# Optimization experiments

Measured on AMD Instinct MI355X. Metric: run time of the kernel, lower is better.

## Reference

```python
import jax, jax.numpy as jnp
import numpy as np
from jax import lax

N, C, H, W = 8, 512, 28, 28
G = 8                     # attention groups
QKP = 32                  # qk_planes = out/groups/2
VP = 64                   # v_planes = branch/groups
BP = 512                  # branch_planes
HW = H * W
EPS = 1e-5                # BatchNorm eps (eval mode, running_mean=0, running_var=1)


def bn(x, gamma, beta, axis=1):
    shape = [1] * x.ndim
    shape[axis] = x.shape[axis]
    g = gamma.reshape(shape)
    b = beta.reshape(shape)
    return x * (g / jnp.sqrt(1.0 + EPS)) + b


def conv2d(x, w, groups=1):
    return lax.conv_general_dilated(
        x, w, (1, 1), 'SAME',
        dimension_numbers=('NCHW', 'OIHW', 'NCHW'),
        feature_group_count=groups)


def setup_inputs() -> dict:
    key = jax.random.key(0)
    ks = jax.random.split(key, 16)
    pe_dim = 2 * QKP + VP  # 128
    inp = {
        'x':        jax.random.normal(ks[0], (N, C, H, W), jnp.float32),
        'qkv_w':    jax.random.normal(ks[1], (BP * 2, C), jnp.float32) * np.sqrt(1.0 / C),
        'g_qkv':    jax.random.normal(ks[2], (BP * 2,), jnp.float32) * 0.1 + 1.0,
        'b_qkv':    jax.random.normal(ks[3], (BP * 2,), jnp.float32) * 0.1,
        'g_sim':    jax.random.normal(ks[4], (G * 3,), jnp.float32) * 0.1 + 1.0,
        'b_sim':    jax.random.normal(ks[5], (G * 3,), jnp.float32) * 0.1,
        'g_out':    jax.random.normal(ks[6], (BP * 2,), jnp.float32) * 0.1 + 1.0,
        'b_out':    jax.random.normal(ks[7], (BP * 2,), jnp.float32) * 0.1,
        'relative': jax.random.normal(ks[8], (pe_dim, 2 * HW - 1), jnp.float32) * np.sqrt(1.0 / VP),
        'xw1':      jax.random.normal(ks[9], (BP, C // G, 3, 3), jnp.float32) * np.sqrt(2.0 / (C // G * 9)),
        'xw2':      jax.random.normal(ks[10], (BP, BP, 1, 1), jnp.float32) * np.sqrt(2.0 / BP),
        'g_x':      jnp.ones((BP,), jnp.float32),
        'b_x':      jnp.zeros((BP,), jnp.float32),
        'rw':       jax.random.normal(ks[11], (BP, BP * 2, 1, 1), jnp.float32) * np.sqrt(2.0 / (BP * 2)),
        'g_r':      jnp.ones((BP,), jnp.float32),
        'b_r':      jnp.zeros((BP,), jnp.float32),
        'pw':       jax.random.normal(ks[12], (BP, BP, 1, 1), jnp.float32) * np.sqrt(2.0 / BP),
        'g_p':      jnp.ones((BP,), jnp.float32),
        'b_p':      jnp.zeros((BP,), jnp.float32),
    }
    return inp


def reference(x, qkv_w, g_qkv, b_qkv, g_sim, b_sim, g_out, b_out, relative,
              xw1, xw2, g_x, b_x, rw, g_r, b_r, pw, g_p, b_p):
    n = x.shape[0]
    # ---- unary branch: grouped 3x3 conv + 1x1 conv + BN ----
    unary = conv2d(x, xw1, groups=G)
    unary = conv2d(unary, xw2)
    unary = bn(unary, g_x, b_x)

    # ---- binary branch (attention over HW tokens) ----
    xf = x.reshape(n, C, HW)
    qkv = jnp.einsum('oc,bci->boi', qkv_w, xf)          # Conv1d k=1
    qkv = bn(qkv, g_qkv, b_qkv)
    qkv = qkv.reshape(n, G, 2 * QKP + VP, HW)
    q = qkv[:, :, :QKP]
    k = qkv[:, :, QKP:2 * QKP]
    v = qkv[:, :, 2 * QKP:]

    # relative position embeddings via index gather: emb[c,i,j] = relative[c, i-j+HW-1]
    idx = jnp.arange(HW)
    rel_idx = idx[:, None] - idx[None, :] + HW - 1      # [HW, HW]
    emb = relative[:, rel_idx]                           # [pe_dim, HW, HW]
    q_emb, k_emb, v_emb = emb[:QKP], emb[QKP:2 * QKP], emb[2 * QKP:]

    qk = jnp.einsum('bgci,bgcj->bgij', q, k)
    qr = jnp.einsum('bgci,cij->bgij', q, q_emb)
    kr = jnp.einsum('bgci,cij->bgij', k, k_emb).swapaxes(2, 3)
    stacked = jnp.concatenate([qk, qr, kr], axis=1)      # [n, 3G, HW, HW]
    stacked = bn(stacked, g_sim, b_sim)
    logits = stacked.reshape(n, 3, G, HW, HW).sum(axis=1)
    sim = jax.nn.softmax(logits, axis=-1)                # softmax over keys j

    sv = jnp.einsum('bgij,bgcj->bgci', sim, v)
    sve = jnp.einsum('bgij,cij->bgci', sim, v_emb)
    stacked_binary = jnp.concatenate([sv, sve], axis=-1).reshape(n, BP * 2, HW)
    stacked_binary = bn(stacked_binary, g_out, b_out)
    binary = stacked_binary.reshape(n, BP, 2, HW).sum(axis=2).reshape(n, BP, H, W)

    # ---- gating / reasoning path ----
    gate_in = jnp.concatenate([unary, binary], axis=1)   # [n, 2*BP, H, W]
    r = jax.nn.relu(gate_in)
    r = jax.nn.relu(bn(conv2d(r, rw), g_r, b_r))
    gate = jax.nn.sigmoid(bn(conv2d(r, pw), g_p, b_p))

    return gate * binary + unary


if __name__ == '__main__':
    out = reference(**setup_inputs())
    print(out.shape, out.dtype)
```

## Files before the change

### kernel.cpp

```cpp
#include <hip/hip_runtime.h>
#include <math.h>


typedef unsigned short u16;
typedef unsigned int u32;
typedef __bf16 bf16x8 __attribute__((ext_vector_type(8)));
typedef float f32x4 __attribute__((ext_vector_type(4)));

#define INVS 0.99999500003749968f
#define MFMA16(a, b, c) __builtin_amdgcn_mfma_f32_16x16x32_bf16(a, b, c, 0, 0, 0)

__device__ inline u16 f2bf(float f) {
  u32 u = __builtin_bit_cast(u32, f);
  return (u16)((u + 0x7fffu + ((u >> 16) & 1u)) >> 16);
}
__device__ inline bf16x8 ld_bf8(const u16* p) {
  int4 v = *reinterpret_cast<const int4*>(p);
  return __builtin_bit_cast(bf16x8, v);
}
__device__ inline bf16x8 pack8(const u16 h[8]) {
  int4 v;
  v.x = (int)((u32)h[0] | ((u32)h[1] << 16));
  v.y = (int)((u32)h[2] | ((u32)h[3] << 16));
  v.z = (int)((u32)h[4] | ((u32)h[5] << 16));
  v.w = (int)((u32)h[6] | ((u32)h[7] << 16));
  return __builtin_bit_cast(bf16x8, v);
}
__device__ inline bf16x8 zero8() {
  int4 z = {0, 0, 0, 0};
  return __builtin_bit_cast(bf16x8, z);
}
__device__ inline float bpermf(float v, int srcl) {
  return __builtin_bit_cast(float,
      __builtin_amdgcn_ds_bpermute(srcl << 2, __builtin_bit_cast(int, v)));
}


__device__ void body_prep(
    int idx, const float* __restrict__ qkv_w, const float* __restrict__ xw2,
    const float* __restrict__ rw, const float* __restrict__ pw,
    const float* __restrict__ xw1, const float* __restrict__ rel,
    u16* __restrict__ Wq, u16* __restrict__ W2, u16* __restrict__ Wr,
    u16* __restrict__ Wp, u16* __restrict__ W1t, u16* __restrict__ relq,
    u16* __restrict__ relk, u16* __restrict__ relv) {
  if (idx < 524288) { Wq[idx] = f2bf(qkv_w[idx]); return; }
  idx -= 524288;
  if (idx < 262144) { W2[idx] = f2bf(xw2[idx]); return; }
  idx -= 262144;
  if (idx < 524288) { Wr[idx] = f2bf(rw[idx]); return; }
  idx -= 524288;
  if (idx < 262144) { Wp[idx] = f2bf(pw[idx]); return; }
  idx -= 262144;
  if (idx < 294912) {
    int gk = idx >> 12, rem = idx & 4095, oc = rem >> 6, ic = rem & 63;
    int g = gk / 9, k9 = gk % 9;
    W1t[idx] = f2bf(xw1[(((g * 64 + oc) * 64) + ic) * 9 + k9]);
    return;
  }
  idx -= 294912;
  if (idx < 51200) {
    int t = idx >> 5, c = idx & 31;
    relq[idx] = (t < 1567) ? f2bf(rel[c * 1567 + t]) : (u16)0;
    return;
  }
  idx -= 51200;
  if (idx < 51200) {
    int t = idx >> 5, c = idx & 31;
    relk[idx] = (t < 1567) ? f2bf(rel[(32 + c) * 1567 + t]) : (u16)0;
    return;
  }
  idx -= 51200;
  if (idx < 102400) {
    int c = idx / 1600, t = idx % 1600;
    relv[idx] = (t < 1567) ? f2bf(rel[(64 + c) * 1567 + t]) : (u16)0;
    return;
  }
}

__device__ void body_transpose(int bx, int by, int bz, const float* __restrict__ x,
                               u16* __restrict__ xT, char* smem) {
  const int b = bz, c0 = by * 64, n0 = bx * 32;
  const int tid = threadIdx.x;
  u16(*tl)[36] = reinterpret_cast<u16(*)[36]>(smem);
#pragma unroll
  for (int h = 0; h < 2; ++h) {
    int cl = (tid >> 3) + h * 32;
    int n4 = (tid & 7) * 4;
    float4 v = {0.f, 0.f, 0.f, 0.f};
    if (n0 + n4 + 3 < 784)
      v = *reinterpret_cast<const float4*>(x + ((size_t)b * 512 + c0 + cl) * 784 + n0 + n4);
    u32 lo = (u32)f2bf(v.x) | ((u32)f2bf(v.y) << 16);
    u32 hi = (u32)f2bf(v.z) | ((u32)f2bf(v.w) << 16);
    *reinterpret_cast<int2*>(&tl[cl][n4]) = make_int2((int)lo, (int)hi);
  }
  __syncthreads();
  int nl = tid >> 3, c8 = (tid & 7) * 8;
  if (n0 + nl < 784) {
    u16 h[8];
#pragma unroll
    for (int e = 0; e < 8; ++e) h[e] = tl[c8 + e][nl];
    *reinterpret_cast<int4*>(xT + ((size_t)b * 784 + n0 + nl) * 512 + c0 + c8) =
        __builtin_bit_cast(int4, pack8(h));
  }
}

__device__ void body_qkv(int bx, int by, int bz,
                         const u16* __restrict__ W, const u16* __restrict__ xT,
                         const float* __restrict__ gq, const float* __restrict__ bq,
                         u16* __restrict__ Qs, u16* __restrict__ Ks,
                         u16* __restrict__ Vs, char* smem) {
  const int b = bz, mt = by, n0 = bx * 112;
  const int tid = threadIdx.x, lane = tid & 63, wave = tid >> 6;
  const int lm = lane & 15, lq = lane >> 4;
  u16* Bl = reinterpret_cast<u16*>(smem);
  f32x4 zf = {0.f, 0.f, 0.f, 0.f};
  f32x4 acc[7];
#pragma unroll
  for (int t = 0; t < 7; ++t) acc[t] = zf;
  const u16* Bb = xT + ((size_t)b * 784 + n0) * 512;
  const u16* Ar = W + (size_t)(mt * 64 + wave * 16 + lm) * 512;
  const int row0 = tid >> 2, seg8 = (tid & 3) * 8;
  const u16* src0 = Bb + (size_t)row0 * 512 + seg8;
  const u16* src1 = src0 + (size_t)64 * 512;
  u16* dst0 = &Bl[row0 * 40 + seg8];
  u16* dst1 = &Bl[(row0 + 64) * 40 + seg8];
  int4 p0 = *reinterpret_cast<const int4*>(src0);
  int4 p1;
  if (tid < 192) p1 = *reinterpret_cast<const int4*>(src1);
  bf16x8 afc = ld_bf8(Ar + lq * 8);
  for (int ks = 0; ks < 16; ++ks) {
    *reinterpret_cast<int4*>(dst0) = p0;
    if (tid < 192) *reinterpret_cast<int4*>(dst1) = p1;
    __syncthreads();
    bf16x8 af = afc;
    if (ks < 15) {
      p0 = *reinterpret_cast<const int4*>(src0 + (ks + 1) * 32);
      if (tid < 192) p1 = *reinterpret_cast<const int4*>(src1 + (ks + 1) * 32);
      afc = ld_bf8(Ar + (ks + 1) * 32 + lq * 8);
    }
#pragma unroll
    for (int t = 0; t < 7; ++t) {
      bf16x8 bf8 = ld_bf8(&Bl[(t * 16 + lm) * 40 + lq * 8]);
      acc[t] = MFMA16(af, bf8, acc[t]);
    }
    __syncthreads();
  }
  const int og = mt * 64 + wave * 16 + lq * 4;
  float sc[4], bi[4];
#pragma unroll
  for (int r = 0; r < 4; ++r) { sc[r] = gq[og + r] * INVS; bi[r] = bq[og + r]; }
  const int g = og >> 7, r128 = og & 127;
  const size_t bg = (size_t)b * 8 + g;
#pragma unroll
  for (int t = 0; t < 7; ++t) {
    int j = n0 + t * 16 + lm;
    u16 h[4];
#pragma unroll
    for (int r = 0; r < 4; ++r) h[r] = f2bf(acc[t][r] * sc[r] + bi[r]);
    if (r128 < 64) {
      u16* dst = (r128 < 32) ? Qs : Ks;
      int c = r128 & 31;
      u32 lo = (u32)h[0] | ((u32)h[1] << 16);
      u32 hi = (u32)h[2] | ((u32)h[3] << 16);
      *reinterpret_cast<int2*>(dst + (bg * 784 + j) * 32 + c) = make_int2((int)lo, (int)hi);
    } else {
      int c = r128 - 64;
#pragma unroll
      for (int r = 0; r < 4; ++r) Vs[(bg * 64 + c + r) * 784 + j] = h[r];
    }
  }
}

__device__ void body_conv1(int bx, int by, int bz, const u16* __restrict__ xT,
                           const u16* __restrict__ W1t, u16* __restrict__ umid,
                           char* smem) {
  const int b = bz, g = by, n0 = bx * 112;
  const int tid = threadIdx.x, lane = tid & 63, wave = tid >> 6;
  const int lm = lane & 15, lq = lane >> 4;
  u16* xl = reinterpret_cast<u16*>(smem);
  for (int u = tid; u < 1360; u += 256) {
    int row = u >> 3, seg = u & 7;
    int ng = n0 - 29 + row;
    int4 v = {0, 0, 0, 0};
    if (ng >= 0 && ng < 784)
      v = *reinterpret_cast<const int4*>(xT + ((size_t)b * 784 + ng) * 512 + g * 64 + seg * 8);
    *reinterpret_cast<int4*>(&xl[row * 72 + seg * 8]) = v;
  }
  __syncthreads();
  f32x4 zf = {0.f, 0.f, 0.f, 0.f};
  f32x4 acc[7];
#pragma unroll
  for (int t = 0; t < 7; ++t) acc[t] = zf;
  const u16* Wg = W1t + (size_t)g * 9 * 4096;
#pragma unroll
  for (int k9 = 0; k9 < 9; ++k9) {
    const int dh = k9 / 3 - 1, dw = k9 % 3 - 1;
#pragma unroll
    for (int ks = 0; ks < 2; ++ks) {
      bf16x8 af = ld_bf8(Wg + (k9 * 64 + wave * 16 + lm) * 64 + ks * 32 + lq * 8);
#pragma unroll
      for (int t = 0; t < 7; ++t) {
        int n = n0 + t * 16 + lm;
        int ww = n % 28 + dw;
        bf16x8 bf8;
        if (ww >= 0 && ww < 28)
          bf8 = ld_bf8(&xl[(t * 16 + lm + dh * 28 + dw + 29) * 72 + ks * 32 + lq * 8]);
        else
          bf8 = zero8();
        acc[t] = MFMA16(af, bf8, acc[t]);
      }
    }
  }
  const int oc4 = g * 64 + wave * 16 + lq * 4;
#pragma unroll
  for (int t = 0; t < 7; ++t) {
    int j = n0 + t * 16 + lm;
    u16 h[4];
#pragma unroll
    for (int r = 0; r < 4; ++r) h[r] = f2bf(acc[t][r]);
    u32 lo = (u32)h[0] | ((u32)h[1] << 16);
    u32 hi = (u32)h[2] | ((u32)h[3] << 16);
    *reinterpret_cast<int2*>(umid + ((size_t)b * 784 + j) * 512 + oc4) = make_int2((int)lo, (int)hi);
  }
}

__device__ void body_x2(int bx, int by, int bz,
                        const u16* __restrict__ W, const u16* __restrict__ Bsrc,
                        const float* __restrict__ gv, const float* __restrict__ bv,
                        float* __restrict__ outT, u16* __restrict__ outTh, char* smem) {
  const int b = bz, mt = by, n0 = bx * 112;
  const int tid = threadIdx.x, lane = tid & 63, wave = tid >> 6;
  const int lm = lane & 15, lq = lane >> 4;
  u16* Bl = reinterpret_cast<u16*>(smem);
  f32x4 zf = {0.f, 0.f, 0.f, 0.f};
  f32x4 acc[7];
#pragma unroll
  for (int t = 0; t < 7; ++t) acc[t] = zf;
  const u16* Bb = Bsrc + ((size_t)b * 784 + n0) * 512;
  const u16* Ar = W + (size_t)(mt * 64 + wave * 16 + lm) * 512;
  for (int ks = 0; ks < 16; ++ks) {
    __syncthreads();
    for (int u = tid; u < 448; u += 256) {
      int row = u >> 2, seg = u & 3;
      int4 v = *reinterpret_cast<const int4*>(Bb + (size_t)row * 512 + ks * 32 + seg * 8);
      *reinterpret_cast<int4*>(&Bl[row * 40 + seg * 8]) = v;
    }
    __syncthreads();
    bf16x8 af = ld_bf8(Ar + ks * 32 + lq * 8);
#pragma unroll
    for (int t = 0; t < 7; ++t) {
      bf16x8 bf8 = ld_bf8(&Bl[(t * 16 + lm) * 40 + lq * 8]);
      acc[t] = MFMA16(af, bf8, acc[t]);
    }
  }
  const int og = mt * 64 + wave * 16 + lq * 4;
  float sc[4], bi[4];
#pragma unroll
  for (int r = 0; r < 4; ++r) { sc[r] = gv[og + r] * INVS; bi[r] = bv[og + r]; }
#pragma unroll
  for (int t = 0; t < 7; ++t) {
    int j = n0 + t * 16 + lm;
    float4 o4;
    o4.x = acc[t][0] * sc[0] + bi[0];
    o4.y = acc[t][1] * sc[1] + bi[1];
    o4.z = acc[t][2] * sc[2] + bi[2];
    o4.w = acc[t][3] * sc[3] + bi[3];
    *reinterpret_cast<float4*>(outT + ((size_t)b * 784 + j) * 512 + og) = o4;
    u32 lo = (u32)f2bf(fmaxf(o4.x, 0.f)) | ((u32)f2bf(fmaxf(o4.y, 0.f)) << 16);
    u32 hi = (u32)f2bf(fmaxf(o4.z, 0.f)) | ((u32)f2bf(fmaxf(o4.w, 0.f)) << 16);
    *reinterpret_cast<int2*>(outTh + ((size_t)b * 784 + j) * 512 + og) = make_int2((int)lo, (int)hi);
  }
}

__device__ void body_attn(int bx, int by, int bz,
                          const u16* __restrict__ Qs, const u16* __restrict__ Ks,
                          const u16* __restrict__ Vs, const u16* __restrict__ relq,
                          const u16* __restrict__ relk, const u16* __restrict__ relv,
                          const float* __restrict__ g_sim, const float* __restrict__ g_out,
                          const float* __restrict__ b_out, float* __restrict__ binT,
                          u16* __restrict__ binTh, char* smem) {
  const int b = bz, g = by, i0 = bx * 16;
  const int tid = threadIdx.x, lane = tid & 63, wave = tid >> 6;
  const int lm = lane & 15, lq = lane >> 4;
  u16* Pl = reinterpret_cast<u16*>(smem);
  float* KRs = reinterpret_cast<float*>(smem + 27936);
  float* WM = reinterpret_cast<float*>(smem + 36640);
  float* rstat = reinterpret_cast<float*>(smem + 36896);
  for (int u = tid; u < 1424; u += 256) {
    int idx = (u < 16) ? u : (16 + ((u - 16) / 88) * 872 + 784 + (u - 16) % 88);
    Pl[idx] = 0;
  }
  const float s0 = g_sim[g] * INVS, s1 = g_sim[8 + g] * INVS, s2 = g_sim[16 + g] * INVS;
  const size_t bg = (size_t)b * 8 + g;
  const u16* Qb = Qs + bg * 784 * 32;
  const u16* Kb = Ks + bg * 784 * 32;
  const u16* Vb = Vs + bg * 64 * 784;
  const bf16x8 aq = ld_bf8(Qb + (i0 + lm) * 32 + lq * 8);
  const f32x4 zf = {0.f, 0.f, 0.f, 0.f};
  float vmax[4] = {-1e30f, -1e30f, -1e30f, -1e30f};
  bf16x8 kfc, bq0c, bq1c, bk0c, bk1c;
  {
    const int j0 = wave * 16;
    const int d0 = 768 + i0 - j0, e0 = 768 + j0 - i0;
    kfc = ld_bf8(Kb + (j0 + lm) * 32 + lq * 8);
    bq0c = ld_bf8(relq + (d0 + lm) * 32 + lq * 8);
    bq1c = ld_bf8(relq + (d0 + 16 + lm) * 32 + lq * 8);
    bk0c = ld_bf8(relk + (e0 + lm) * 32 + lq * 8);
    bk1c = ld_bf8(relk + (e0 + 16 + lm) * 32 + lq * 8);
  }
  int jt = wave;
  for (int rr = 0; rr < 13; ++rr) {
    const int jtn = jt + 4;
    bf16x8 kfn = kfc, bq0n = bq0c, bq1n = bq1c, bk0n = bk0c, bk1n = bk1c;
    if (jtn < 49) {
      const int j0n = jtn * 16;
      const int d0 = 768 + i0 - j0n, e0 = 768 + j0n - i0;
      kfn = ld_bf8(Kb + (j0n + lm) * 32 + lq * 8);
      bq0n = ld_bf8(relq + (d0 + lm) * 32 + lq * 8);
      bq1n = ld_bf8(relq + (d0 + 16 + lm) * 32 + lq * 8);
      bk0n = ld_bf8(relk + (e0 + lm) * 32 + lq * 8);
      bk1n = ld_bf8(relk + (e0 + 16 + lm) * 32 + lq * 8);
    }
    if (jt < 49) {
      const int j0 = jt * 16;
      f32x4 aqk = MFMA16(aq, kfc, zf);
      f32x4 q0 = MFMA16(aq, bq0c, zf);
      f32x4 q1 = MFMA16(aq, bq1c, zf);
      f32x4 k0 = MFMA16(kfc, bk0c, zf);
      f32x4 k1 = MFMA16(kfc, bk1c, zf);
#pragma unroll
      for (int r = 0; r < 4; ++r) {
        int m = lq * 4 + r;
        KRs[(wave * 16 + m) * 34 + lm] = k0[r];
        KRs[(wave * 16 + m) * 34 + 16 + lm] = k1[r];
      }
#pragma unroll
      for (int r = 0; r < 4; ++r) {
        int m = lq * 4 + r, n = lm;
        int c = m - n + 15;
        int srcl = (c & 15) | (lane & 48);
        float t0 = bpermf(q0[r], srcl), t1 = bpermf(q1[r], srcl);
        float qv = (c & 16) ? t1 : t0;
        float kv = KRs[(wave * 16 + n) * 34 + (n - m + 15)];
        float val = aqk[r] * s0 + qv * s1 + kv * s2;
        vmax[r] = fmaxf(vmax[r], val);
        _Float16 hv = (_Float16)val;
        Pl[16 + m * 872 + j0 + n] = __builtin_bit_cast(u16, hv);
      }
    }
    jt = jtn;
    kfc = kfn; bq0c = bq0n; bq1c = bq1n; bk0c = bk0n; bk1c = bk1n;
  }
#pragma unroll
  for (int r = 0; r < 4; ++r) {
#pragma unroll
    for (int d = 1; d < 16; d <<= 1) vmax[r] = fmaxf(vmax[r], __shfl_xor(vmax[r], d, 64));
  }
  if (lm == 0) {
#pragma unroll
    for (int r = 0; r < 4; ++r) WM[wave * 16 + lq * 4 + r] = vmax[r];
  }
  __syncthreads();
  {
    const int row = tid >> 4, sub = tid & 15;
    u16* Pr = &Pl[16 + row * 872];
    float gmax = fmaxf(fmaxf(WM[row], WM[16 + row]), fmaxf(WM[32 + row], WM[48 + row]));
    float sm = 0.f;
    for (int k = 0; k < 49; ++k) {
      int j = sub + 16 * k;
      _Float16 hv = __builtin_bit_cast(_Float16, Pr[j]);
      float e = __expf((float)hv - gmax);
      sm += e;
      Pr[j] = f2bf(e);
    }
#pragma unroll
    for (int d = 1; d < 16; d <<= 1) sm += __shfl_xor(sm, d, 64);
    if (sub == 0) rstat[row] = 1.0f / sm;
  }
  __syncthreads();
  f32x4 accV = zf, accE = zf;
  const int coff = wave * 16;
  const u16* Vr = Vb + (size_t)(coff + lm) * 784;
  const u16* Rr = relv + (size_t)(coff + lm) * 1600 + i0;
  const u16* Prow = &Pl[16 + lm * 872];
  for (int ks = 0; ks < 25; ++ks) {
    bf16x8 ap = ld_bf8(Prow + ks * 32 + lq * 8);
    bf16x8 bv = ld_bf8(Vr + ks * 32 + lq * 8);
    accV = MFMA16(ap, bv, accV);
    const int base = 783 + lm - ks * 32 - lq * 8;
    u16 h[8];
#pragma unroll
    for (int e = 0; e < 8; ++e) h[e] = Prow[base - e];
    bf16x8 ash = pack8(h);
    bf16x8 br = ld_bf8(Rr + ks * 32 + lq * 8);
    accE = MFMA16(ash, br, accE);
  }
  const int c = coff + lm;
  const int oi = g * 128 + 2 * c;
  const float so0 = g_out[oi] * INVS, bo0 = b_out[oi];
  const float so1 = g_out[oi + 1] * INVS, bo1 = b_out[oi + 1];
#pragma unroll
  for (int r = 0; r < 4; ++r) {
    int row = lq * 4 + r;
    float rl = rstat[row];
    float val = accV[r] * rl * so0 + bo0 + accE[r] * rl * so1 + bo1;
    size_t ofs = ((size_t)b * 784 + i0 + row) * 512 + g * 64 + c;
    binT[ofs] = val;
    binTh[ofs] = f2bf(fmaxf(val, 0.f));
  }
}


__global__ __launch_bounds__(256) void k_pt(
    const float* __restrict__ x, u16* __restrict__ xT,
    const float* __restrict__ qkv_w, const float* __restrict__ xw2,
    const float* __restrict__ rw, const float* __restrict__ pw,
    const float* __restrict__ xw1, const float* __restrict__ rel,
    u16* __restrict__ Wq, u16* __restrict__ W2, u16* __restrict__ Wr,
    u16* __restrict__ Wp, u16* __restrict__ W1t, u16* __restrict__ relq,
    u16* __restrict__ relk, u16* __restrict__ relv) {
  __shared__ __align__(16) char smem[4608];
  const int bid = blockIdx.x;
  if (bid < 1600) {
    body_transpose(bid % 25, (bid / 25) % 8, bid / 200, x, xT, smem);
  } else {
    body_prep((bid - 1600) * 256 + threadIdx.x, qkv_w, xw2, rw, pw, xw1, rel,
              Wq, W2, Wr, Wp, W1t, relq, relk, relv);
  }
}

__global__ __launch_bounds__(256) void k_qc(
    const u16* __restrict__ Wq, const u16* __restrict__ xT,
    const float* __restrict__ gq, const float* __restrict__ bq,
    u16* __restrict__ Qs, u16* __restrict__ Ks, u16* __restrict__ Vs,
    const u16* __restrict__ W1t, u16* __restrict__ umid) {
  __shared__ __align__(16) char smem[24480];
  const int bid = blockIdx.x;
  if (bid < 448) {
    body_conv1(bid % 7, (bid / 7) % 8, bid / 56, xT, W1t, umid, smem);
  } else {
    const int q = bid - 448;
    body_qkv(q % 7, (q / 7) % 16, q / 112, Wq, xT, gq, bq, Qs, Ks, Vs, smem);
  }
}

__global__ __launch_bounds__(256) void k_ax(
    const u16* __restrict__ W2, const u16* __restrict__ umid,
    const float* __restrict__ g_x, const float* __restrict__ b_x,
    float* __restrict__ unT, u16* __restrict__ unTh,
    const u16* __restrict__ Qs, const u16* __restrict__ Ks, const u16* __restrict__ Vs,
    const u16* __restrict__ relq, const u16* __restrict__ relk,
    const u16* __restrict__ relv, const float* __restrict__ g_sim,
    const float* __restrict__ g_out, const float* __restrict__ b_out,
    float* __restrict__ binT, u16* __restrict__ binTh) {
  __shared__ __align__(16) char smem[36960];
  const int bid = blockIdx.x;
  if (bid < 448) {
    body_x2(bid % 7, (bid / 7) % 8, bid / 56, W2, umid, g_x, b_x, unT, unTh, smem);
  } else {
    const int a = bid - 448;
    body_attn(a % 49, (a / 49) % 8, a / 392, Qs, Ks, Vs, relq, relk, relv,
              g_sim, g_out, b_out, binT, binTh, smem);
  }
}

__global__ __launch_bounds__(256) void k_gemm_rw(
    const u16* __restrict__ W, const u16* __restrict__ unTh, const u16* __restrict__ binTh,
    const float* __restrict__ gv, const float* __restrict__ bv, u16* __restrict__ rT) {
  const int b = blockIdx.z, mt = blockIdx.y, n0 = blockIdx.x * 112;
  const int tid = threadIdx.x, lane = tid & 63, wave = tid >> 6;
  const int lm = lane & 15, lq = lane >> 4;
  __shared__ __align__(16) u16 Bl[112 * 40];
  f32x4 zf = {0.f, 0.f, 0.f, 0.f};
  f32x4 acc[7];
#pragma unroll
  for (int t = 0; t < 7; ++t) acc[t] = zf;
  const u16* Ar = W + (size_t)(mt * 64 + wave * 16 + lm) * 1024;
  const int row0 = tid >> 2, seg8 = (tid & 3) * 8;
  const size_t off0 = ((size_t)b * 784 + n0 + row0) * 512 + seg8;
  const size_t off1 = off0 + (size_t)64 * 512;
  u16* dst0 = &Bl[row0 * 40 + seg8];
  u16* dst1 = &Bl[(row0 + 64) * 40 + seg8];
  int4 p0 = *reinterpret_cast<const int4*>(unTh + off0);
  int4 p1;
  if (tid < 192) p1 = *reinterpret_cast<const int4*>(unTh + off1);
  bf16x8 afc = ld_bf8(Ar + lq * 8);
  for (int ks = 0; ks < 32; ++ks) {
    *reinterpret_cast<int4*>(dst0) = p0;
    if (tid < 192) *reinterpret_cast<int4*>(dst1) = p1;
    __syncthreads();
    bf16x8 af = afc;
    if (ks < 31) {
      const int ksn = ks + 1;
      const u16* sb = (ksn < 16) ? unTh : binTh;
      const int k0 = (ksn & 15) * 32;
      p0 = *reinterpret_cast<const int4*>(sb + off0 + k0);
      if (tid < 192) p1 = *reinterpret_cast<const int4*>(sb + off1 + k0);
      afc = ld_bf8(Ar + ksn * 32 + lq * 8);
    }
#pragma unroll
    for (int t = 0; t < 7; ++t) {
      bf16x8 bf8 = ld_bf8(&Bl[(t * 16 + lm) * 40 + lq * 8]);
      acc[t] = MFMA16(af, bf8, acc[t]);
    }
    __syncthreads();
  }
  const int og = mt * 64 + wave * 16 + lq * 4;
  float sc[4], bi[4];
#pragma unroll
  for (int r = 0; r < 4; ++r) { sc[r] = gv[og + r] * INVS; bi[r] = bv[og + r]; }
#pragma unroll
  for (int t = 0; t < 7; ++t) {
    int j = n0 + t * 16 + lm;
    u16 h[4];
#pragma unroll
    for (int r = 0; r < 4; ++r) h[r] = f2bf(fmaxf(acc[t][r] * sc[r] + bi[r], 0.f));
    u32 lo = (u32)h[0] | ((u32)h[1] << 16);
    u32 hi = (u32)h[2] | ((u32)h[3] << 16);
    *reinterpret_cast<int2*>(rT + ((size_t)b * 784 + j) * 512 + og) = make_int2((int)lo, (int)hi);
  }
}

__global__ __launch_bounds__(256) void k_gemm_pw(
    const u16* __restrict__ W, const u16* __restrict__ rT,
    const float* __restrict__ gv, const float* __restrict__ bv,
    const float* __restrict__ binT, const float* __restrict__ unT,
    float* __restrict__ out) {
  const int b = blockIdx.z, mt = blockIdx.y, n0 = blockIdx.x * 112;
  const int tid = threadIdx.x, lane = tid & 63, wave = tid >> 6;
  const int lm = lane & 15, lq = lane >> 4;
  __shared__ __align__(16) u16 Bl[112 * 40];
  f32x4 zf = {0.f, 0.f, 0.f, 0.f};
  f32x4 acc[7];
#pragma unroll
  for (int t = 0; t < 7; ++t) acc[t] = zf;
  const u16* Bb = rT + ((size_t)b * 784 + n0) * 512;
  const u16* Ar = W + (size_t)(mt * 64 + wave * 16 + lm) * 512;
  const int row0 = tid >> 2, seg8 = (tid & 3) * 8;
  const u16* src0 = Bb + (size_t)row0 * 512 + seg8;
  const u16* src1 = src0 + (size_t)64 * 512;
  u16* dst0 = &Bl[row0 * 40 + seg8];
  u16* dst1 = &Bl[(row0 + 64) * 40 + seg8];
  int4 p0 = *reinterpret_cast<const int4*>(src0);
  int4 p1;
  if (tid < 192) p1 = *reinterpret_cast<const int4*>(src1);
  bf16x8 afc = ld_bf8(Ar + lq * 8);
  for (int ks = 0; ks < 16; ++ks) {
    *reinterpret_cast<int4*>(dst0) = p0;
    if (tid < 192) *reinterpret_cast<int4*>(dst1) = p1;
    __syncthreads();
    bf16x8 af = afc;
    if (ks < 15) {
      p0 = *reinterpret_cast<const int4*>(src0 + (ks + 1) * 32);
      if (tid < 192) p1 = *reinterpret_cast<const int4*>(src1 + (ks + 1) * 32);
      afc = ld_bf8(Ar + (ks + 1) * 32 + lq * 8);
    }
#pragma unroll
    for (int t = 0; t < 7; ++t) {
      bf16x8 bf8 = ld_bf8(&Bl[(t * 16 + lm) * 40 + lq * 8]);
      acc[t] = MFMA16(af, bf8, acc[t]);
    }
    __syncthreads();
  }
  const int og = mt * 64 + wave * 16 + lq * 4;
  float sc[4], bi[4];
#pragma unroll
  for (int r = 0; r < 4; ++r) { sc[r] = gv[og + r] * INVS; bi[r] = bv[og + r]; }
#pragma unroll
  for (int t = 0; t < 7; ++t) {
    int j = n0 + t * 16 + lm;
    float4 bin4 = *reinterpret_cast<const float4*>(binT + ((size_t)b * 784 + j) * 512 + og);
    float4 un4 = *reinterpret_cast<const float4*>(unT + ((size_t)b * 784 + j) * 512 + og);
    float binv[4] = {bin4.x, bin4.y, bin4.z, bin4.w};
    float unv[4] = {un4.x, un4.y, un4.z, un4.w};
#pragma unroll
    for (int r = 0; r < 4; ++r) {
      float gt = 1.f / (1.f + __expf(-(acc[t][r] * sc[r] + bi[r])));
      out[((size_t)b * 512 + og + r) * 784 + j] = gt * binv[r] + unv[r];
    }
  }
}

extern "C" void kernel_launch(void* const* d_in, const int* in_sizes, int n_in,
                              void* d_out, int out_size, void* d_ws, size_t ws_size,
                              hipStream_t stream) {
  const float* x = (const float*)d_in[0];
  const float* qkv_w = (const float*)d_in[1];
  const float* g_qkv = (const float*)d_in[2];
  const float* b_qkv = (const float*)d_in[3];
  const float* g_sim = (const float*)d_in[4];
  const float* g_out = (const float*)d_in[6];
  const float* b_out = (const float*)d_in[7];
  const float* relative = (const float*)d_in[8];
  const float* xw1 = (const float*)d_in[9];
  const float* xw2 = (const float*)d_in[10];
  const float* g_x = (const float*)d_in[11];
  const float* b_x = (const float*)d_in[12];
  const float* rw = (const float*)d_in[13];
  const float* g_r = (const float*)d_in[14];
  const float* b_r = (const float*)d_in[15];
  const float* pw = (const float*)d_in[16];
  const float* g_p = (const float*)d_in[17];
  const float* b_p = (const float*)d_in[18];

  char* p = (char*)d_ws;
  auto take = [&](size_t n) { char* q = p; p += (n + 255) & ~(size_t)255; return q; };
  u16* xT = (u16*)take((size_t)8 * 784 * 512 * 2);
  u16* Wq = (u16*)take((size_t)1024 * 512 * 2);
  u16* W2 = (u16*)take((size_t)512 * 512 * 2);
  u16* Wr = (u16*)take((size_t)512 * 1024 * 2);
  u16* Wp = (u16*)take((size_t)512 * 512 * 2);
  u16* W1t = (u16*)take((size_t)294912 * 2);
  u16* relq = (u16*)take((size_t)51200 * 2);
  u16* relk = (u16*)take((size_t)51200 * 2);
  u16* relv = (u16*)take((size_t)102400 * 2);
  u16* Qs = (u16*)take((size_t)8 * 8 * 784 * 32 * 2);
  u16* Ks = (u16*)take((size_t)8 * 8 * 784 * 32 * 2);
  u16* Vs = (u16*)take(((size_t)8 * 8 * 64 * 784 + 64) * 2);
  u16* umid = (u16*)take((size_t)8 * 784 * 512 * 2);
  float* unT = (float*)take((size_t)8 * 784 * 512 * 4);
  float* binT = (float*)take((size_t)8 * 784 * 512 * 4);
  u16* rT = (u16*)take((size_t)8 * 784 * 512 * 2);
  u16* unTh = (u16*)take((size_t)8 * 784 * 512 * 2);
  u16* binTh = (u16*)take((size_t)8 * 784 * 512 * 2);

  k_pt<<<dim3(9696), dim3(256), 0, stream>>>(x, xT, qkv_w, xw2, rw, pw, xw1, relative,
                                             Wq, W2, Wr, Wp, W1t, relq, relk, relv);
  k_qc<<<dim3(1344), dim3(256), 0, stream>>>(Wq, xT, g_qkv, b_qkv, Qs, Ks, Vs, W1t, umid);
  k_ax<<<dim3(3584), dim3(256), 0, stream>>>(W2, umid, g_x, b_x, unT, unTh, Qs, Ks, Vs,
                                             relq, relk, relv, g_sim, g_out, b_out,
                                             binT, binTh);
  k_gemm_rw<<<dim3(7, 8, 8), dim3(256), 0, stream>>>(Wr, unTh, binTh, g_r, b_r, rT);
  k_gemm_pw<<<dim3(7, 8, 8), dim3(256), 0, stream>>>(Wp, rT, g_p, b_p, binT, unT,
                                                     (float*)d_out);
}
```

Before: 290.7 us.

## Store unary/binary intermediates once as bf16 and apply relu in the gate GEMM loader

The unary and binary activations were each written twice, as an fp32 copy and a bf16 relu copy. They are now written once as signed bf16, the relu moves into the rw GEMM's shared-memory staging through a bitmask, and the final gating epilogue reads bf16 instead of fp32. The softmax exponent pass is also vectorised to 8-element LDS accesses, and k_ax gets a launch-bounds occupancy hint. This cuts global write and read traffic between kernels, at the cost of bf16 precision in the residual terms of the final output.

Result: no change. 296.0 us (+1.8%).

```diff
diff --git a/kernel.cpp b/kernel.cpp
--- a/kernel.cpp
+++ b/kernel.cpp
@@ -13,6 +13,10 @@
 __device__ inline u16 f2bf(float f) {
   u32 u = __builtin_bit_cast(u32, f);
   return (u16)((u + 0x7fffu + ((u >> 16) & 1u)) >> 16);
+}
+__device__ inline float bf2f(u16 h) {
+  u32 u = ((u32)h) << 16;
+  return __builtin_bit_cast(float, u);
 }
 __device__ inline bf16x8 ld_bf8(const u16* p) {
   int4 v = *reinterpret_cast<const int4*>(p);
@@ -33,6 +37,16 @@
 __device__ inline float bpermf(float v, int srcl) {
   return __builtin_bit_cast(float,
       __builtin_amdgcn_ds_bpermute(srcl << 2, __builtin_bit_cast(int, v)));
+}
+__device__ inline int4 relu8(int4 v) {
+  u32* w = reinterpret_cast<u32*>(&v);
+#pragma unroll
+  for (int k = 0; k < 4; ++k) {
+    u32 x = w[k];
+    u32 s = (x >> 15) & 0x00010001u;
+    w[k] = x & ((0x00010001u - s) * 0xFFFFu);
+  }
+  return v;
 }
 
 
@@ -227,7 +241,7 @@
 __device__ void body_x2(int bx, int by, int bz,
                         const u16* __restrict__ W, const u16* __restrict__ Bsrc,
                         const float* __restrict__ gv, const float* __restrict__ bv,
-                        float* __restrict__ outT, u16* __restrict__ outTh, char* smem) {
+                        u16* __restrict__ outB, char* smem) {
   const int b = bz, mt = by, n0 = bx * 112;
   const int tid = threadIdx.x, lane = tid & 63, wave = tid >> 6;
   const int lm = lane & 15, lq = lane >> 4;
@@ -260,15 +274,12 @@
 #pragma unroll
   for (int t = 0; t < 7; ++t) {
     int j = n0 + t * 16 + lm;
-    float4 o4;
-    o4.x = acc[t][0] * sc[0] + bi[0];
-    o4.y = acc[t][1] * sc[1] + bi[1];
-    o4.z = acc[t][2] * sc[2] + bi[2];
-    o4.w = acc[t][3] * sc[3] + bi[3];
-    *reinterpret_cast<float4*>(outT + ((size_t)b * 784 + j) * 512 + og) = o4;
-    u32 lo = (u32)f2bf(fmaxf(o4.x, 0.f)) | ((u32)f2bf(fmaxf(o4.y, 0.f)) << 16);
-    u32 hi = (u32)f2bf(fmaxf(o4.z, 0.f)) | ((u32)f2bf(fmaxf(o4.w, 0.f)) << 16);
-    *reinterpret_cast<int2*>(outTh + ((size_t)b * 784 + j) * 512 + og) = make_int2((int)lo, (int)hi);
+    u16 h[4];
+#pragma unroll
+    for (int r = 0; r < 4; ++r) h[r] = f2bf(acc[t][r] * sc[r] + bi[r]);
+    u32 lo = (u32)h[0] | ((u32)h[1] << 16);
+    u32 hi = (u32)h[2] | ((u32)h[3] << 16);
+    *reinterpret_cast<int2*>(outB + ((size_t)b * 784 + j) * 512 + og) = make_int2((int)lo, (int)hi);
   }
 }
 
@@ -277,8 +288,8 @@
                           const u16* __restrict__ Vs, const u16* __restrict__ relq,
                           const u16* __restrict__ relk, const u16* __restrict__ relv,
                           const float* __restrict__ g_sim, const float* __restrict__ g_out,
-                          const float* __restrict__ b_out, float* __restrict__ binT,
-                          u16* __restrict__ binTh, char* smem) {
+                          const float* __restrict__ b_out, u16* __restrict__ binB,
+                          char* smem) {
   const int b = bz, g = by, i0 = bx * 16;
   const int tid = threadIdx.x, lane = tid & 63, wave = tid >> 6;
   const int lm = lane & 15, lq = lane >> 4;
@@ -366,12 +377,17 @@
     u16* Pr = &Pl[16 + row * 872];
     float gmax = fmaxf(fmaxf(WM[row], WM[16 + row]), fmaxf(WM[32 + row], WM[48 + row]));
     float sm = 0.f;
-    for (int k = 0; k < 49; ++k) {
-      int j = sub + 16 * k;
-      _Float16 hv = __builtin_bit_cast(_Float16, Pr[j]);
-      float e = __expf((float)hv - gmax);
-      sm += e;
-      Pr[j] = f2bf(e);
+    for (int c = sub; c < 98; c += 16) {
+      int4 v = *reinterpret_cast<int4*>(&Pr[c * 8]);
+      u16* hh = reinterpret_cast<u16*>(&v);
+      u16 oo[8];
+#pragma unroll
+      for (int e = 0; e < 8; ++e) {
+        float ev = __expf((float)__builtin_bit_cast(_Float16, hh[e]) - gmax);
+        sm += ev;
+        oo[e] = f2bf(ev);
+      }
+      *reinterpret_cast<int4*>(&Pr[c * 8]) = __builtin_bit_cast(int4, pack8(oo));
     }
 #pragma unroll
     for (int d = 1; d < 16; d <<= 1) sm += __shfl_xor(sm, d, 64);
@@ -404,9 +420,7 @@
     int row = lq * 4 + r;
     float rl = rstat[row];
     float val = accV[r] * rl * so0 + bo0 + accE[r] * rl * so1 + bo1;
-    size_t ofs = ((size_t)b * 784 + i0 + row) * 512 + g * 64 + c;
-    binT[ofs] = val;
-    binTh[ofs] = f2bf(fmaxf(val, 0.f));
+    binB[((size_t)b * 784 + i0 + row) * 512 + g * 64 + c] = f2bf(val);
   }
 }
 
@@ -444,28 +458,28 @@
   }
 }
 
-__global__ __launch_bounds__(256) void k_ax(
+__global__ __launch_bounds__(256, 8) void k_ax(
     const u16* __restrict__ W2, const u16* __restrict__ umid,
     const float* __restrict__ g_x, const float* __restrict__ b_x,
-    float* __restrict__ unT, u16* __restrict__ unTh,
+    u16* __restrict__ unB,
     const u16* __restrict__ Qs, const u16* __restrict__ Ks, const u16* __restrict__ Vs,
     const u16* __restrict__ relq, const u16* __restrict__ relk,
     const u16* __restrict__ relv, const float* __restrict__ g_sim,
     const float* __restrict__ g_out, const float* __restrict__ b_out,
-    float* __restrict__ binT, u16* __restrict__ binTh) {
+    u16* __restrict__ binB) {
   __shared__ __align__(16) char smem[36960];
   const int bid = blockIdx.x;
   if (bid < 448) {
-    body_x2(bid % 7, (bid / 7) % 8, bid / 56, W2, umid, g_x, b_x, unT, unTh, smem);
+    body_x2(bid % 7, (bid / 7) % 8, bid / 56, W2, umid, g_x, b_x, unB, smem);
   } else {
     const int a = bid - 448;
     body_attn(a % 49, (a / 49) % 8, a / 392, Qs, Ks, Vs, relq, relk, relv,
-              g_sim, g_out, b_out, binT, binTh, smem);
+              g_sim, g_out, b_out, binB, smem);
   }
 }
 
 __global__ __launch_bounds__(256) void k_gemm_rw(
-    const u16* __restrict__ W, const u16* __restrict__ unTh, const u16* __restrict__ binTh,
+    const u16* __restrict__ W, const u16* __restrict__ unB, const u16* __restrict__ binB,
     const float* __restrict__ gv, const float* __restrict__ bv, u16* __restrict__ rT) {
   const int b = blockIdx.z, mt = blockIdx.y, n0 = blockIdx.x * 112;
   const int tid = threadIdx.x, lane = tid & 63, wave = tid >> 6;
@@ -481,18 +495,18 @@
   const size_t off1 = off0 + (size_t)64 * 512;
   u16* dst0 = &Bl[row0 * 40 + seg8];
   u16* dst1 = &Bl[(row0 + 64) * 40 + seg8];
-  int4 p0 = *reinterpret_cast<const int4*>(unTh + off0);
+  int4 p0 = *reinterpret_cast<const int4*>(unB + off0);
   int4 p1;
-  if (tid < 192) p1 = *reinterpret_cast<const int4*>(unTh + off1);
+  if (tid < 192) p1 = *reinterpret_cast<const int4*>(unB + off1);
   bf16x8 afc = ld_bf8(Ar + lq * 8);
   for (int ks = 0; ks < 32; ++ks) {
-    *reinterpret_cast<int4*>(dst0) = p0;
-    if (tid < 192) *reinterpret_cast<int4*>(dst1) = p1;
+    *reinterpret_cast<int4*>(dst0) = relu8(p0);
+    if (tid < 192) *reinterpret_cast<int4*>(dst1) = relu8(p1);
     __syncthreads();
     bf16x8 af = afc;
     if (ks < 31) {
       const int ksn = ks + 1;
-      const u16* sb = (ksn < 16) ? unTh : binTh;
+      const u16* sb = (ksn < 16) ? unB : binB;
       const int k0 = (ksn & 15) * 32;
       p0 = *reinterpret_cast<const int4*>(sb + off0 + k0);
       if (tid < 192) p1 = *reinterpret_cast<const int4*>(sb + off1 + k0);
@@ -524,7 +538,7 @@
 __global__ __launch_bounds__(256) void k_gemm_pw(
     const u16* __restrict__ W, const u16* __restrict__ rT,
     const float* __restrict__ gv, const float* __restrict__ bv,
-    const float* __restrict__ binT, const float* __restrict__ unT,
+    const u16* __restrict__ binB, const u16* __restrict__ unB,
     float* __restrict__ out) {
   const int b = blockIdx.z, mt = blockIdx.y, n0 = blockIdx.x * 112;
   const int tid = threadIdx.x, lane = tid & 63, wave = tid >> 6;
@@ -569,14 +583,15 @@
 #pragma unroll
   for (int t = 0; t < 7; ++t) {
     int j = n0 + t * 16 + lm;
-    float4 bin4 = *reinterpret_cast<const float4*>(binT + ((size_t)b * 784 + j) * 512 + og);
-    float4 un4 = *reinterpret_cast<const float4*>(unT + ((size_t)b * 784 + j) * 512 + og);
-    float binv[4] = {bin4.x, bin4.y, bin4.z, bin4.w};
-    float unv[4] = {un4.x, un4.y, un4.z, un4.w};
+    size_t ofs = ((size_t)b * 784 + j) * 512 + og;
+    int2 b2 = *reinterpret_cast<const int2*>(binB + ofs);
+    int2 u2 = *reinterpret_cast<const int2*>(unB + ofs);
+    const u16* bh = reinterpret_cast<const u16*>(&b2);
+    const u16* uh = reinterpret_cast<const u16*>(&u2);
 #pragma unroll
     for (int r = 0; r < 4; ++r) {
       float gt = 1.f / (1.f + __expf(-(acc[t][r] * sc[r] + bi[r])));
-      out[((size_t)b * 512 + og + r) * 784 + j] = gt * binv[r] + unv[r];
+      out[((size_t)b * 512 + og + r) * 784 + j] = gt * bf2f(bh[r]) + bf2f(uh[r]);
     }
   }
 }
@@ -618,19 +633,16 @@
   u16* Ks = (u16*)take((size_t)8 * 8 * 784 * 32 * 2);
   u16* Vs = (u16*)take(((size_t)8 * 8 * 64 * 784 + 64) * 2);
   u16* umid = (u16*)take((size_t)8 * 784 * 512 * 2);
-  float* unT = (float*)take((size_t)8 * 784 * 512 * 4);
-  float* binT = (float*)take((size_t)8 * 784 * 512 * 4);
+  u16* unB = (u16*)take((size_t)8 * 784 * 512 * 2);
+  u16* binB = (u16*)take((size_t)8 * 784 * 512 * 2);
   u16* rT = (u16*)take((size_t)8 * 784 * 512 * 2);
-  u16* unTh = (u16*)take((size_t)8 * 784 * 512 * 2);
-  u16* binTh = (u16*)take((size_t)8 * 784 * 512 * 2);
 
   k_pt<<<dim3(9696), dim3(256), 0, stream>>>(x, xT, qkv_w, xw2, rw, pw, xw1, relative,
                                              Wq, W2, Wr, Wp, W1t, relq, relk, relv);
   k_qc<<<dim3(1344), dim3(256), 0, stream>>>(Wq, xT, g_qkv, b_qkv, Qs, Ks, Vs, W1t, umid);
-  k_ax<<<dim3(3584), dim3(256), 0, stream>>>(W2, umid, g_x, b_x, unT, unTh, Qs, Ks, Vs,
-                                             relq, relk, relv, g_sim, g_out, b_out,
-                                             binT, binTh);
-  k_gemm_rw<<<dim3(7, 8, 8), dim3(256), 0, stream>>>(Wr, unTh, binTh, g_r, b_r, rT);
-  k_gemm_pw<<<dim3(7, 8, 8), dim3(256), 0, stream>>>(Wp, rT, g_p, b_p, binT, unT,
+  k_ax<<<dim3(3584), dim3(256), 0, stream>>>(W2, umid, g_x, b_x, unB, Qs, Ks, Vs,
+                                             relq, relk, relv, g_sim, g_out, b_out, binB);
+  k_gemm_rw<<<dim3(7, 8, 8), dim3(256), 0, stream>>>(Wr, unB, binB, g_r, b_r, rT);
+  k_gemm_pw<<<dim3(7, 8, 8), dim3(256), 0, stream>>>(Wp, rT, g_p, b_p, binB, unB,
                                                      (float*)d_out);
 }
```
